# Optimization experiments

Hardware: AMD Instinct MI355X
Metric: run time of the kernel (lower is better)

Reference implementation:

```python
import jax, jax.numpy as jnp
import numpy as np

DIV_VAL = 11.313708498984761  # sqrt(128), the softmax temperature used as div_val


def setup_inputs() -> dict:
    key = jax.random.key(0)
    kq, kk, kv = jax.random.split(key, 3)
    B, Lq, Lk, D = 16, 4096, 4096, 128
    return {
        "query": jax.random.normal(kq, (B, Lq, D), dtype=jnp.float32),
        "key": jax.random.normal(kk, (B, Lk, D), dtype=jnp.float32),
        "value": jax.random.normal(kv, (B, Lk, D), dtype=jnp.float32),
    }


def reference(query, key, value):
    # qk = Q @ K^T, scaled by 1/div_val  -> [B, Lq, Lk]
    scaled_qk = jnp.einsum("bqd,bkd->bqk", query, key) / DIV_VAL
    # numerically stable softmax over last axis; dropout is identity (eval / p=0)
    attn = jax.nn.softmax(scaled_qk, axis=-1)
    # output = attn @ V -> [B, Lq, Dv]
    return jnp.einsum("bqk,bkd->bqd", attn, value)
```

## Files before the change

### kernel.cpp

```cpp
#include <hip/hip_runtime.h>

#define B_  16
#define L_  4096
#define D_  128
#define NT  (L_ / 64)

typedef __attribute__((ext_vector_type(8)))  __bf16 bf16x8;
typedef __attribute__((ext_vector_type(2)))  __bf16 bf16x2;
typedef __attribute__((ext_vector_type(16))) float  f32x16;
typedef __attribute__((ext_vector_type(4)))  float  f32x4;
typedef __attribute__((ext_vector_type(4)))  int    i32x4;
typedef __attribute__((ext_vector_type(8)))  unsigned short u16x8;
typedef __attribute__((ext_vector_type(4)))  unsigned short u16x4;

#ifndef __has_builtin
#define __has_builtin(x) 0
#endif
#if __has_builtin(__builtin_amdgcn_permlane32_swap)
#define HAVE_PLSWAP 1
#else
#define HAVE_PLSWAP 0
#endif

__device__ __forceinline__ unsigned short f2bf(float f){
  unsigned u = __builtin_bit_cast(unsigned, f);
  u += 0x7fffu + ((u >> 16) & 1u);
  return (unsigned short)(u >> 16);
}

__device__ __forceinline__ int packbf(float a, float b){
  bf16x2 t; t[0] = (__bf16)a; t[1] = (__bf16)b;
  return __builtin_bit_cast(int, t);
}

__device__ __forceinline__ void gload16(const void* g, void* l){
  __builtin_amdgcn_global_load_lds(
      (const __attribute__((address_space(1))) unsigned int*)g,
      (__attribute__((address_space(3))) unsigned int*)l, 16, 0, 0);
}

__global__ void cvt_bf16_kernel(const float* __restrict__ in,
                                unsigned short* __restrict__ out, int n8){
  int i = blockIdx.x * blockDim.x + threadIdx.x;
  if (i >= n8) return;
  const float4* p = reinterpret_cast<const float4*>(in) + (size_t)i * 2;
  float4 a = p[0], b = p[1];
  u16x8 o;
  o[0]=f2bf(a.x); o[1]=f2bf(a.y); o[2]=f2bf(a.z); o[3]=f2bf(a.w);
  o[4]=f2bf(b.x); o[5]=f2bf(b.y); o[6]=f2bf(b.z); o[7]=f2bf(b.w);
  reinterpret_cast<u16x8*>(out)[i] = o;
}

__global__ void transpose_v_kernel(const float* __restrict__ V,
                                   unsigned short* __restrict__ Vt){
  __shared__ unsigned short tile[64][65];
  const int k0 = blockIdx.x * 64, d0 = blockIdx.y * 64, b = blockIdx.z;
  const int tr = threadIdx.x >> 4, tc = threadIdx.x & 15;
  const float* src = V + ((size_t)b * L_ + k0) * D_ + d0;
#pragma unroll
  for (int p = 0; p < 4; ++p){
    int kl = p * 16 + tr;
    float4 v = *reinterpret_cast<const float4*>(src + (size_t)kl * D_ + tc * 4);
    tile[kl][tc*4+0] = f2bf(v.x);
    tile[kl][tc*4+1] = f2bf(v.y);
    tile[kl][tc*4+2] = f2bf(v.z);
    tile[kl][tc*4+3] = f2bf(v.w);
  }
  __syncthreads();
  unsigned short* dst = Vt + (size_t)b * D_ * L_ + (size_t)d0 * L_ + k0;
#pragma unroll
  for (int p = 0; p < 4; ++p){
    int dl = p * 16 + tr;
    u16x4 o;
    o[0] = tile[tc*4+0][dl];
    o[1] = tile[tc*4+1][dl];
    o[2] = tile[tc*4+2][dl];
    o[3] = tile[tc*4+3][dl];
    *reinterpret_cast<u16x4*>(dst + (size_t)dl * L_ + tc * 4) = o;
  }
}

__device__ __forceinline__ bf16x8 mkchunk(float a0,float a1,float a2,float a3,
                                          float a4,float a5,float a6,float a7,
                                          int hi){
  int x0 = packbf(a0,a1), x1 = packbf(a2,a3);
  int x2 = packbf(a4,a5), x3 = packbf(a6,a7);
  int W0, W1, W2, W3;
#if HAVE_PLSWAP
  {
    auto r = __builtin_amdgcn_permlane32_swap((unsigned)x0, (unsigned)x2, false, false);
    W0 = (int)r[0]; W2 = (int)r[1];
  }
  {
    auto r = __builtin_amdgcn_permlane32_swap((unsigned)x1, (unsigned)x3, false, false);
    W1 = (int)r[0]; W3 = (int)r[1];
  }
  (void)hi;
#else
  int y0 = __shfl_xor(x0, 32), y1 = __shfl_xor(x1, 32);
  int y2 = __shfl_xor(x2, 32), y3 = __shfl_xor(x3, 32);
  W0 = hi ? y2 : x0;  W1 = hi ? y3 : x1;
  W2 = hi ? x2 : y0;  W3 = hi ? x3 : y1;
#endif
  i32x4 ww; ww[0]=W0; ww[1]=W1; ww[2]=W2; ww[3]=W3;
  return __builtin_bit_cast(bf16x8, ww);
}

__global__ __launch_bounds__(256, 2)
void attn_kernel(const float* __restrict__ Q,
                 const unsigned short* __restrict__ Kb,
                 const unsigned short* __restrict__ Vt,
                 float* __restrict__ out){
  __shared__ char smem[65536];
  char* Klds = smem;
  char* Vlds = smem + 32768;

  const int tid = threadIdx.x;
  const int w = tid >> 6, l = tid & 63;
  const int row = l & 31, hi = l >> 5;
  const int swz = (row & 7) << 4;
  const int b = blockIdx.x, qt = blockIdx.y;

  const float* qptr = Q + ((size_t)b * L_ + (size_t)qt * 128 + w * 32 + row) * D_;
  bf16x8 qf[8];
#pragma unroll
  for (int c = 0; c < 8; ++c){
    float4 a = *reinterpret_cast<const float4*>(qptr + c * 16 + hi * 8);
    float4 bb = *reinterpret_cast<const float4*>(qptr + c * 16 + hi * 8 + 4);
    u16x8 o;
    o[0]=f2bf(a.x); o[1]=f2bf(a.y); o[2]=f2bf(a.z); o[3]=f2bf(a.w);
    o[4]=f2bf(bb.x); o[5]=f2bf(bb.y); o[6]=f2bf(bb.z); o[7]=f2bf(bb.w);
    qf[c] = __builtin_bit_cast(bf16x8, o);
  }

  const char* Kg = (const char*)(Kb + (size_t)b * L_ * D_);
  const char* Vg = (const char*)(Vt + (size_t)b * (size_t)D_ * L_);

  f32x16 o[4];
#pragma unroll
  for (int n = 0; n < 4; ++n)
#pragma unroll
    for (int i = 0; i < 16; ++i) o[n][i] = 0.f;
  float m = -1e30f, ln = 0.f;

  constexpr float SCALE_L2E = 1.4426950408889634f / 11.313708498984761f;
  constexpr float THR = 11.0f;

  auto STAGE = [&](int buf, int t){
    const int kv0 = t * 64;
#pragma unroll
    for (int j = 0; j < 4; ++j){
      int idx = j * 256 + tid;
      int kr = idx >> 4, kc = (idx & 15) << 4;
      gload16(Kg + (size_t)(kv0 + kr) * 256 + (kc ^ ((kr & 7) << 4)),
              Klds + buf * 16384 + idx * 16);
    }
#pragma unroll
    for (int j = 0; j < 4; ++j){
      int idx = j * 256 + tid;
      int vr = idx >> 3, vc = (idx & 7) << 4;
      gload16(Vg + (size_t)vr * (L_ * 2) + (size_t)kv0 * 2 + (vc ^ ((vr & 7) << 4)),
              Vlds + buf * 16384 + idx * 16);
    }
  };

  STAGE(0, 0);
  __syncthreads();
  int cur = 0;

  for (int t = 0; t < NT; ++t){
    if (t + 1 < NT) STAGE(cur ^ 1, t + 1);

    const char* Kc = Klds + cur * 16384;
    const char* Vc = Vlds + cur * 16384;

    f32x16 s0 = {0.f,0,0,0, 0,0,0,0, 0,0,0,0, 0,0,0,0};
    f32x16 s1 = {0.f,0,0,0, 0,0,0,0, 0,0,0,0, 0,0,0,0};
    __builtin_amdgcn_s_setprio(1);
#pragma unroll
    for (int c = 0; c < 8; ++c){
      bf16x8 kf0 = *(const bf16x8*)(Kc + row * 256 + ((c * 32 + hi * 16) ^ swz));
      bf16x8 kf1 = *(const bf16x8*)(Kc + (row + 32) * 256 + ((c * 32 + hi * 16) ^ swz));
      s0 = __builtin_amdgcn_mfma_f32_32x32x16_bf16(kf0, qf[c], s0, 0, 0, 0);
      s1 = __builtin_amdgcn_mfma_f32_32x32x16_bf16(kf1, qf[c], s1, 0, 0, 0);
    }
    __builtin_amdgcn_s_setprio(0);

    float mx = -1e30f;
#pragma unroll
    for (int i = 0; i < 16; ++i) mx = fmaxf(mx, fmaxf(s0[i], s1[i]));
    mx *= SCALE_L2E;
    mx = fmaxf(mx, __shfl_xor(mx, 32));

    if (!__all(mx <= m + THR)){
      float mn = fmaxf(m, mx);
      float corr = __builtin_amdgcn_exp2f(m - mn);
      m = mn; ln *= corr;
#pragma unroll
      for (int n = 0; n < 4; ++n)
#pragma unroll
        for (int i = 0; i < 16; ++i) o[n][i] *= corr;
    }

    f32x16 p0, p1;
#pragma unroll
    for (int i = 0; i < 16; ++i){
      p0[i] = __builtin_amdgcn_exp2f(fmaf(s0[i], SCALE_L2E, -m));
      p1[i] = __builtin_amdgcn_exp2f(fmaf(s1[i], SCALE_L2E, -m));
    }
    float ps = 0.f;
#pragma unroll
    for (int i = 0; i < 16; ++i) ps += p0[i] + p1[i];
    ln += ps;

    bf16x8 pa0 = mkchunk(p0[0],p0[1],p0[2],p0[3],p0[4],p0[5],p0[6],p0[7], hi);
    bf16x8 pa1 = mkchunk(p0[8],p0[9],p0[10],p0[11],p0[12],p0[13],p0[14],p0[15], hi);
    bf16x8 pa2 = mkchunk(p1[0],p1[1],p1[2],p1[3],p1[4],p1[5],p1[6],p1[7], hi);
    bf16x8 pa3 = mkchunk(p1[8],p1[9],p1[10],p1[11],p1[12],p1[13],p1[14],p1[15], hi);

    __builtin_amdgcn_s_setprio(1);
#pragma unroll
    for (int n = 0; n < 4; ++n){
      const int vrow = n * 32 + row;
      bf16x8 vf0 = *(const bf16x8*)(Vc + vrow * 128 + ((0 * 32 + hi * 16) ^ swz));
      bf16x8 vf1 = *(const bf16x8*)(Vc + vrow * 128 + ((1 * 32 + hi * 16) ^ swz));
      bf16x8 vf2 = *(const bf16x8*)(Vc + vrow * 128 + ((2 * 32 + hi * 16) ^ swz));
      bf16x8 vf3 = *(const bf16x8*)(Vc + vrow * 128 + ((3 * 32 + hi * 16) ^ swz));
      o[n] = __builtin_amdgcn_mfma_f32_32x32x16_bf16(vf0, pa0, o[n], 0, 0, 0);
      o[n] = __builtin_amdgcn_mfma_f32_32x32x16_bf16(vf1, pa1, o[n], 0, 0, 0);
      o[n] = __builtin_amdgcn_mfma_f32_32x32x16_bf16(vf2, pa2, o[n], 0, 0, 0);
      o[n] = __builtin_amdgcn_mfma_f32_32x32x16_bf16(vf3, pa3, o[n], 0, 0, 0);
    }
    __builtin_amdgcn_s_setprio(0);

    __syncthreads();
    cur ^= 1;
  }

  float lt = ln + __shfl_xor(ln, 32);
  float inv = 1.0f / lt;
  float* outp = out + ((size_t)b * L_ + (size_t)qt * 128 + w * 32 + row) * D_;
#pragma unroll
  for (int n = 0; n < 4; ++n)
#pragma unroll
    for (int rq = 0; rq < 4; ++rq){
      f32x4 v4;
      v4[0] = o[n][rq*4+0] * inv;
      v4[1] = o[n][rq*4+1] * inv;
      v4[2] = o[n][rq*4+2] * inv;
      v4[3] = o[n][rq*4+3] * inv;
      *reinterpret_cast<f32x4*>(outp + n * 32 + rq * 8 + hi * 4) = v4;
    }
}

extern "C" void kernel_launch(void* const* d_in, const int* in_sizes, int n_in,
                              void* d_out, int out_size, void* d_ws, size_t ws_size,
                              hipStream_t stream){
  const float* Q = (const float*)d_in[0];
  const float* K = (const float*)d_in[1];
  const float* V = (const float*)d_in[2];
  float* out = (float*)d_out;

  const size_t NE = (size_t)B_ * L_ * D_;
  unsigned short* kb = (unsigned short*)d_ws;
  unsigned short* vt = kb + NE;

  int n8 = (int)(NE / 8);
  cvt_bf16_kernel<<<dim3(n8 / 256), 256, 0, stream>>>(K, kb, n8);
  transpose_v_kernel<<<dim3(L_ / 64, D_ / 64, B_), 256, 0, stream>>>(V, vt);
  attn_kernel<<<dim3(B_, L_ / 128), 256, 0, stream>>>(Q, kb, vt, out);
}
```

Measured before the change: 200.4 us.

## Read K fragments directly from global, fold softmax scale into K conversion, 512-thread blocks

K tiles are no longer staged in LDS. Each wave now loads its K MFMA fragments straight from global memory, unswizzled, which relies on L2 and L1 for reuse, and LDS holds only V double buffers (32KB). The log2(e)/sqrt(d) scale is folded into the K bf16 conversion kernel, so the inner loop drops the FMA before exp2 and the multiply on the max. Blocks grow to 512 threads covering 256 query rows, which halves the grid and raises reuse of the V tile per LDS load. The risk is higher global-load latency on the QK path with no LDS prefetch for K, and register pressure under launch_bounds(512,2).

```diff
diff --git a/kernel.cpp b/kernel.cpp
--- a/kernel.cpp
+++ b/kernel.cpp
@@ -40,14 +40,15 @@
 }
 
 __global__ void cvt_bf16_kernel(const float* __restrict__ in,
-                                unsigned short* __restrict__ out, int n8){
+                                unsigned short* __restrict__ out, int n8,
+                                float scale){
   int i = blockIdx.x * blockDim.x + threadIdx.x;
   if (i >= n8) return;
   const float4* p = reinterpret_cast<const float4*>(in) + (size_t)i * 2;
   float4 a = p[0], b = p[1];
   u16x8 o;
-  o[0]=f2bf(a.x); o[1]=f2bf(a.y); o[2]=f2bf(a.z); o[3]=f2bf(a.w);
-  o[4]=f2bf(b.x); o[5]=f2bf(b.y); o[6]=f2bf(b.z); o[7]=f2bf(b.w);
+  o[0]=f2bf(a.x*scale); o[1]=f2bf(a.y*scale); o[2]=f2bf(a.z*scale); o[3]=f2bf(a.w*scale);
+  o[4]=f2bf(b.x*scale); o[5]=f2bf(b.y*scale); o[6]=f2bf(b.z*scale); o[7]=f2bf(b.w*scale);
   reinterpret_cast<u16x8*>(out)[i] = o;
 }
 
@@ -106,14 +107,13 @@
   return __builtin_bit_cast(bf16x8, ww);
 }
 
-__global__ __launch_bounds__(256, 2)
+__global__ __launch_bounds__(512, 2)
 void attn_kernel(const float* __restrict__ Q,
                  const unsigned short* __restrict__ Kb,
                  const unsigned short* __restrict__ Vt,
                  float* __restrict__ out){
-  __shared__ char smem[65536];
-  char* Klds = smem;
-  char* Vlds = smem + 32768;
+  __shared__ char smem[32768];
+  char* Vlds = smem;
 
   const int tid = threadIdx.x;
   const int w = tid >> 6, l = tid & 63;
@@ -121,14 +121,14 @@
   const int swz = (row & 7) << 4;
   const int b = blockIdx.x, qt = blockIdx.y;
 
-  const float* qptr = Q + ((size_t)b * L_ + (size_t)qt * 128 + w * 32 + row) * D_;
+  const float* qptr = Q + ((size_t)b * L_ + (size_t)qt * 256 + w * 32 + row) * D_;
   bf16x8 qf[8];
 #pragma unroll
   for (int c = 0; c < 8; ++c){
-    float4 a = *reinterpret_cast<const float4*>(qptr + c * 16 + hi * 8);
+    float4 a  = *reinterpret_cast<const float4*>(qptr + c * 16 + hi * 8);
     float4 bb = *reinterpret_cast<const float4*>(qptr + c * 16 + hi * 8 + 4);
     u16x8 o;
-    o[0]=f2bf(a.x); o[1]=f2bf(a.y); o[2]=f2bf(a.z); o[3]=f2bf(a.w);
+    o[0]=f2bf(a.x);  o[1]=f2bf(a.y);  o[2]=f2bf(a.z);  o[3]=f2bf(a.w);
     o[4]=f2bf(bb.x); o[5]=f2bf(bb.y); o[6]=f2bf(bb.z); o[7]=f2bf(bb.w);
     qf[c] = __builtin_bit_cast(bf16x8, o);
   }
@@ -143,21 +143,13 @@
     for (int i = 0; i < 16; ++i) o[n][i] = 0.f;
   float m = -1e30f, ln = 0.f;
 
-  constexpr float SCALE_L2E = 1.4426950408889634f / 11.313708498984761f;
   constexpr float THR = 11.0f;
 
   auto STAGE = [&](int buf, int t){
     const int kv0 = t * 64;
 #pragma unroll
-    for (int j = 0; j < 4; ++j){
-      int idx = j * 256 + tid;
-      int kr = idx >> 4, kc = (idx & 15) << 4;
-      gload16(Kg + (size_t)(kv0 + kr) * 256 + (kc ^ ((kr & 7) << 4)),
-              Klds + buf * 16384 + idx * 16);
-    }
-#pragma unroll
-    for (int j = 0; j < 4; ++j){
-      int idx = j * 256 + tid;
+    for (int j = 0; j < 2; ++j){
+      int idx = j * 512 + tid;
       int vr = idx >> 3, vc = (idx & 7) << 4;
       gload16(Vg + (size_t)vr * (L_ * 2) + (size_t)kv0 * 2 + (vc ^ ((vr & 7) << 4)),
               Vlds + buf * 16384 + idx * 16);
@@ -171,16 +163,18 @@
   for (int t = 0; t < NT; ++t){
     if (t + 1 < NT) STAGE(cur ^ 1, t + 1);
 
-    const char* Kc = Klds + cur * 16384;
+    const char* Kt = Kg + (size_t)t * 64 * 256;
     const char* Vc = Vlds + cur * 16384;
 
     f32x16 s0 = {0.f,0,0,0, 0,0,0,0, 0,0,0,0, 0,0,0,0};
     f32x16 s1 = {0.f,0,0,0, 0,0,0,0, 0,0,0,0, 0,0,0,0};
+    const char* k0p = Kt + row * 256 + hi * 16;
+    const char* k1p = k0p + 32 * 256;
     __builtin_amdgcn_s_setprio(1);
 #pragma unroll
     for (int c = 0; c < 8; ++c){
-      bf16x8 kf0 = *(const bf16x8*)(Kc + row * 256 + ((c * 32 + hi * 16) ^ swz));
-      bf16x8 kf1 = *(const bf16x8*)(Kc + (row + 32) * 256 + ((c * 32 + hi * 16) ^ swz));
+      bf16x8 kf0 = *(const bf16x8*)(k0p + c * 32);
+      bf16x8 kf1 = *(const bf16x8*)(k1p + c * 32);
       s0 = __builtin_amdgcn_mfma_f32_32x32x16_bf16(kf0, qf[c], s0, 0, 0, 0);
       s1 = __builtin_amdgcn_mfma_f32_32x32x16_bf16(kf1, qf[c], s1, 0, 0, 0);
     }
@@ -189,7 +183,6 @@
     float mx = -1e30f;
 #pragma unroll
     for (int i = 0; i < 16; ++i) mx = fmaxf(mx, fmaxf(s0[i], s1[i]));
-    mx *= SCALE_L2E;
     mx = fmaxf(mx, __shfl_xor(mx, 32));
 
     if (!__all(mx <= m + THR)){
@@ -197,20 +190,19 @@
       float corr = __builtin_amdgcn_exp2f(m - mn);
       m = mn; ln *= corr;
 #pragma unroll
-      for (int n = 0; n < 4; ++n)
-#pragma unroll
-        for (int i = 0; i < 16; ++i) o[n][i] *= corr;
+      for (int n = 0; n < 4; ++n) o[n] *= corr;
     }
 
     f32x16 p0, p1;
 #pragma unroll
     for (int i = 0; i < 16; ++i){
-      p0[i] = __builtin_amdgcn_exp2f(fmaf(s0[i], SCALE_L2E, -m));
-      p1[i] = __builtin_amdgcn_exp2f(fmaf(s1[i], SCALE_L2E, -m));
-    }
+      p0[i] = __builtin_amdgcn_exp2f(s0[i] - m);
+      p1[i] = __builtin_amdgcn_exp2f(s1[i] - m);
+    }
+    f32x16 pt = p0 + p1;
     float ps = 0.f;
 #pragma unroll
-    for (int i = 0; i < 16; ++i) ps += p0[i] + p1[i];
+    for (int i = 0; i < 16; ++i) ps += pt[i];
     ln += ps;
 
     bf16x8 pa0 = mkchunk(p0[0],p0[1],p0[2],p0[3],p0[4],p0[5],p0[6],p0[7], hi);
@@ -239,7 +231,7 @@
 
   float lt = ln + __shfl_xor(ln, 32);
   float inv = 1.0f / lt;
-  float* outp = out + ((size_t)b * L_ + (size_t)qt * 128 + w * 32 + row) * D_;
+  float* outp = out + ((size_t)b * L_ + (size_t)qt * 256 + w * 32 + row) * D_;
 #pragma unroll
   for (int n = 0; n < 4; ++n)
 #pragma unroll
@@ -265,8 +257,9 @@
   unsigned short* kb = (unsigned short*)d_ws;
   unsigned short* vt = kb + NE;
 
+  const float SCALE_L2E = 1.4426950408889634f / 11.313708498984761f;
   int n8 = (int)(NE / 8);
-  cvt_bf16_kernel<<<dim3(n8 / 256), 256, 0, stream>>>(K, kb, n8);
+  cvt_bf16_kernel<<<dim3(n8 / 256), 256, 0, stream>>>(K, kb, n8, SCALE_L2E);
   transpose_v_kernel<<<dim3(L_ / 64, D_ / 64, B_), 256, 0, stream>>>(V, vt);
-  attn_kernel<<<dim3(B_, L_ / 128), 256, 0, stream>>>(Q, kb, vt, out);
-}
+  attn_kernel<<<dim3(B_, L_ / 256), 512, 0, stream>>>(Q, kb, vt, out);
+}
```

Result: slower. 357.3 us (+78.3%).
